# Optimization experiments

Measured on AMD Instinct MI355X. Metric: run time of the kernel, lower is better.

The kernel has to match this reference:

```python
import jax, jax.numpy as jnp
import numpy as np

THRESH = 0.1          # affinity threshold from init_kwargs
SCALES = (1, 2, 4, 8, 16)  # dyadic diffusion scales 2^0..2^4


def compute_dist(X):
    # X: [N, d] -> squared-euclidean pairwise distances via Gram matrix
    G = X @ X.T
    dg = jnp.diag(G)
    return dg[None, :] + dg[:, None] - 2.0 * G


def _diffuse(P, F):
    # returns [P^1 F, P^2 F, P^4 F, P^8 F, P^16 F] via 16 sequential applies
    outs = []
    cur = F
    for step in range(1, SCALES[-1] + 1):
        cur = P @ cur
        if step in SCALES:
            outs.append(cur)
    return outs


def _wavelet_bank(P, F):
    # lazy diffusion wavelets: psi_0 = I - P, psi_j = P^{2^{j-1}} - P^{2^j}
    lows = [F] + _diffuse(P, F)            # t = 0,1,2,4,8,16
    psis = [lows[j] - lows[j + 1] for j in range(len(lows) - 1)]  # 5 wavelets
    return psis, lows[-1]                  # (wavelet coeffs, low-pass P^16 F)


def _gwt_features(X):
    # X: [N, d] reweighted point cloud -> [N, 16*d] scattering features
    N, d = X.shape
    W = jnp.exp(-compute_dist(X) / 10.0)
    W = jnp.where(W < THRESH, jnp.zeros_like(W), W)   # sparsify affinity
    deg = W.sum(axis=1, keepdims=True)                # self-loop w=1 => deg>=1
    P = 0.5 * (jnp.eye(N, dtype=X.dtype) + W / deg)   # lazy random walk
    psis, low = _wavelet_bank(P, X)
    firsts = [jnp.abs(p) for p in psis]
    U = jnp.concatenate(firsts, axis=1)               # [N, 5*d] diffuse all at once
    psis2, _ = _wavelet_bank(P, U)
    # second order: |psi_{j2} |psi_{j1} x|| only for j2 > j1 (10 pairs)
    seconds = [jnp.abs(psis2[j2][:, : j2 * d]) for j2 in range(1, len(psis2))]
    return jnp.concatenate([low] + firsts + seconds, axis=1)  # [N, (1+5+10)*d]


def setup_inputs() -> dict:
    key = jax.random.key(0)
    k1, k2 = jax.random.split(key)
    point_clouds = jax.random.normal(k1, (4, 2048, 3), dtype=jnp.float32)
    alphas = jax.random.uniform(k2, (4, 3), dtype=jnp.float32)  # learned param
    return {"point_clouds": point_clouds, "alphas": alphas}


def reference(point_clouds, alphas):
    # point_clouds: [B, N, d]; alphas: [K, d]
    Xb = point_clouds[:, None, :, :] * alphas[None, :, None, :]  # [B, K, N, d]
    feats = jax.vmap(jax.vmap(_gwt_features))(Xb)                # [B, K, N, 16d]
    # per-cloud: cat over K along feature dim then mean over nodes == mean then flatten
    return feats.mean(axis=2).reshape(feats.shape[0], -1)        # [B, K*16*d]
```

## Files before the change

### kernel.cpp

```cpp
#include <hip/hip_runtime.h>
#include <hip/hip_bf16.h>


#define NN 2048
#define NPAIR 16

typedef _Float16 half8 __attribute__((ext_vector_type(8)));
typedef _Float16 f16x2 __attribute__((ext_vector_type(2)));
typedef float f32x4 __attribute__((ext_vector_type(4)));

extern "C" __device__ f16x2 __ocml_exp2_2f16(f16x2);

#define C2F 0.28853900817779268f
#define CWF -0.14426950408889634f
#define NL2T 3.3219280948873623f

__global__ __launch_bounds__(256) void initpack_k(const float* __restrict__ pc,
                                                  const float* __restrict__ alphas,
                                                  float* __restrict__ Xs,
                                                  _Float16* __restrict__ XT,
                                                  _Float16* __restrict__ Xp) {
    int gid = blockIdx.x * 256 + threadIdx.x;
    if (gid >= NPAIR * NN) return;
    int p = gid >> 11, i = gid & (NN - 1);
    int b = p >> 2, k = p & 3;
    const float* pcr = pc + ((size_t)b * NN + i) * 3;
    const float* al  = alphas + k * 3;
    float x = pcr[0] * al[0], y = pcr[1] * al[1], z = pcr[2] * al[2];
    float q = CWF * (x * x + y * y + z * z);
    float4 o; o.x = x; o.y = y; o.z = z; o.w = q;
    ((float4*)Xs)[gid] = o;
    _Float16* xt = XT + (size_t)p * 16 * NN + i;
    xt[0 * NN] = (_Float16)x;
    xt[1 * NN] = (_Float16)y;
    xt[2 * NN] = (_Float16)z;
    xt[3 * NN] = (_Float16)1.0f;
#pragma unroll
    for (int n = 4; n < 16; ++n) xt[n * NN] = (_Float16)0.f;
    _Float16* xp = Xp + ((size_t)p * 1024 + (i >> 1)) * 8 + (i & 1);
    xp[0] = (_Float16)x; xp[2] = (_Float16)y;
    xp[4] = (_Float16)z; xp[6] = (_Float16)q;
}

template<bool FIRST, bool BUILDU>
__global__ __launch_bounds__(512, 8)
void apply_k(const float* __restrict__ Xs, const _Float16* __restrict__ Xp,
             float* __restrict__ ihd,
             const _Float16* __restrict__ cur, _Float16* __restrict__ out,
             float* __restrict__ lvl, int t,
             const float* __restrict__ LT1u) {
    __shared__ __align__(16) float smem[4352];
    const int tid  = threadIdx.x;
    const int lane = tid & 63;
    const int wv   = tid >> 6;
    const int p    = blockIdx.y;
    const int m0   = blockIdx.x * 32;
    const int idx16 = lane & 15, quad = lane >> 4;

    {
        const float4* src = (const float4*)(Xp + (size_t)p * 8192);
        float4* dst = (float4*)smem;
        dst[tid]       = src[tid];
        dst[tid + 512] = src[tid + 512];
    }
    __syncthreads();

    f16x2 qi2[2], xx2[2], xy2[2], xz2[2];
#pragma unroll
    for (int s = 0; s < 2; ++s) {
        float4 v = *(const float4*)(Xs + ((size_t)p * NN + m0 + s * 16 + idx16) * 4);
        _Float16 q = (_Float16)(v.w + NL2T);
        _Float16 x = (_Float16)(C2F * v.x);
        _Float16 y = (_Float16)(C2F * v.y);
        _Float16 z = (_Float16)(C2F * v.z);
        qi2[s] = (f16x2){q, q}; xx2[s] = (f16x2){x, x};
        xy2[s] = (f16x2){y, y}; xz2[s] = (f16x2){z, z};
    }
    const f16x2 SC2 = (f16x2){(_Float16)32768.f, (_Float16)32768.f};

    const _Float16* bp = cur + ((size_t)p * 16 + idx16) * NN + wv * 256 + quad * 8;
    f32x4 acc[2] = {{0.f,0.f,0.f,0.f},{0.f,0.f,0.f,0.f}};

    for (int kc = 0; kc < 8; ++kc) {
        const int pb = wv * 128 + kc * 16 + quad * 4;
        half8 bf = *(const half8*)(bp + kc * 32);
        union { f16x2 h2[4]; half8 h8; } af[2];
#pragma unroll
        for (int jp = 0; jp < 4; ++jp) {
            union { float4 f; f16x2 h[4]; } e;
            e.f = ((const float4*)smem)[pb + jp];
#pragma unroll
            for (int s = 0; s < 2; ++s) {
                f16x2 tv = qi2[s] + e.h[3];
                tv = __builtin_elementwise_fma(xx2[s], e.h[0], tv);
                tv = __builtin_elementwise_fma(xy2[s], e.h[1], tv);
                tv = __builtin_elementwise_fma(xz2[s], e.h[2], tv);
                f16x2 u = __builtin_elementwise_min(tv, tv * SC2);
                af[s].h2[jp] = __ocml_exp2_2f16(u);
            }
        }
#pragma unroll
        for (int s = 0; s < 2; ++s)
            acc[s] = __builtin_amdgcn_mfma_f32_16x16x32_f16(af[s].h8, bf, acc[s], 0, 0, 0);
    }

    const int n  = tid >> 5;
    const int rr = tid & 31;
    const int s2 = rr >> 4, mloc = rr & 15;
    const int base = s2 * 256 + (mloc >> 2) * 64 + (mloc & 3);
    const int row = m0 + rr;
    float ihEff;
    if (!FIRST) ihEff = 0.1f * ihd[p * NN + row];

    __syncthreads();
#pragma unroll
    for (int s = 0; s < 2; ++s)
        *(f32x4*)&smem[wv * 512 + s * 256 + lane * 4] = acc[s];
    __syncthreads();

    float sum = 0.f;
#pragma unroll
    for (int g = 0; g < 8; ++g) sum += smem[g * 512 + base + n * 4];
    if (FIRST) {
        float deg10 = 0.f;
#pragma unroll
        for (int g = 0; g < 8; ++g) deg10 += smem[g * 512 + base + 12];
        float ih = 5.0f / deg10;
        if (n == 3) ihd[p * NN + row] = ih;
        ihEff = 0.1f * ih;
    }
    float cv = (float)cur[((size_t)p * 16 + n) * NN + row];
    float o1v = 0.5f * cv + ihEff * sum;
    if (lvl) lvl[(((size_t)p * 5 + t) * 16 + n) * NN + row] = o1v;

    if (!BUILDU) {
        out[((size_t)p * 16 + n) * NN + row] = (_Float16)o1v;
    } else {
        if (n < 3) smem[4096 + n * 32 + rr] = o1v;
        __syncthreads();
        float oval = o1v;
        if (n >= 4) {
            const int u = n - 4, jw = u / 3, c = u - 3 * jw;
            float a = (jw == 0) ? Xs[((size_t)p * NN + row) * 4 + c]
                                : LT1u[(((size_t)p * 5 + (jw - 1)) * 16 + c) * NN + row];
            float bb = (jw == 3) ? smem[4096 + c * 32 + rr]
                                 : LT1u[(((size_t)p * 5 + jw) * 16 + c) * NN + row];
            oval = fabsf(a - bb);
        }
        out[((size_t)p * 16 + n) * NN + row] = (_Float16)oval;
    }
}

__global__ __launch_bounds__(64) void reduce_k(const float* __restrict__ Xs,
                                               const float* __restrict__ LT1,
                                               const float* __restrict__ LT2,
                                               float* __restrict__ out) {
    int f = blockIdx.x, p = blockIdx.y, lane = threadIdx.x;
    const float* l1 = LT1 + (size_t)p * 5 * 16 * NN;
    const float* l2 = LT2 + (size_t)p * 5 * 16 * NN;
    float s = 0.f;
    for (int m = lane; m < NN; m += 64) {
        float v;
        if (f < 3) {
            v = l2[((size_t)3 * 16 + f) * NN + m];
        } else if (f < 18) {
            int j = (f - 3) / 3, c = (f - 3) % 3;
            float a = (j == 0) ? Xs[((size_t)p * NN + m) * 4 + c]
                               : l1[((size_t)(j - 1) * 16 + c) * NN + m];
            float b = (j < 4) ? l1[((size_t)j * 16 + c) * NN + m]
                              : l2[((size_t)3 * 16 + c) * NN + m];
            v = fabsf(a - b);
        } else {
            int gg = f - 18, j2, uc;
            if (gg < 3)       { j2 = 1; uc = gg; }
            else if (gg < 9)  { j2 = 2; uc = gg - 3; }
            else if (gg < 18) { j2 = 3; uc = gg - 9; }
            else              { j2 = 4; uc = gg - 18; }
            v = fabsf(l2[((size_t)(j2 - 1) * 16 + uc + 4) * NN + m]
                    - l2[((size_t)j2 * 16 + uc + 4) * NN + m]);
        }
        s += v;
    }
#pragma unroll
    for (int off = 32; off > 0; off >>= 1) s += __shfl_down(s, off, 64);
    if (lane == 0) out[p * 48 + f] = s * (1.0f / NN);
}

extern "C" void kernel_launch(void* const* d_in, const int* in_sizes, int n_in,
                              void* d_out, int out_size, void* d_ws, size_t ws_size,
                              hipStream_t stream) {
    const float* pc     = (const float*)d_in[0];
    const float* alphas = (const float*)d_in[1];
    float* outp = (float*)d_out;

    char* base = (char*)d_ws;
    size_t off = 0;
    auto carve = [&](size_t bytes) -> void* {
        void* r = base + off;
        off = (off + bytes + 255) & ~(size_t)255;
        return r;
    };
    float*     Xs  = (float*)carve((size_t)NPAIR * NN * 4 * sizeof(float));
    _Float16*  Xp  = (_Float16*)carve((size_t)NPAIR * 1024 * 8 * 2);
    float*     ihd = (float*)carve((size_t)NPAIR * NN * sizeof(float));
    _Float16*  XT  = (_Float16*)carve((size_t)NPAIR * 16 * NN * 2);
    _Float16*  pA  = (_Float16*)carve((size_t)NPAIR * 16 * NN * 2);
    _Float16*  pB  = (_Float16*)carve((size_t)NPAIR * 16 * NN * 2);
    float*     LT1 = (float*)carve((size_t)NPAIR * 5 * 16 * NN * sizeof(float));
    float*     LT2 = (float*)carve((size_t)NPAIR * 5 * 16 * NN * sizeof(float));

    dim3 gridA(NN / 32, NPAIR);

    initpack_k<<<dim3((NPAIR * NN) / 256), 256, 0, stream>>>(pc, alphas, Xs, XT, Xp);

    const _Float16* c1 = XT;
    int slot = 0;
    for (int step = 1; step <= 8; ++step) {
        _Float16* o1 = (c1 == pA) ? pB : pA;
        bool sv = (step & (step - 1)) == 0;
        float* lv = sv ? LT1 : nullptr;
        if (step == 1)
            apply_k<true, false><<<gridA, 512, 0, stream>>>(Xs, Xp, ihd,
                c1, o1, lv, slot, nullptr);
        else if (step == 8)
            apply_k<false, true><<<gridA, 512, 0, stream>>>(Xs, Xp, ihd,
                c1, o1, lv, slot, LT1);
        else
            apply_k<false, false><<<gridA, 512, 0, stream>>>(Xs, Xp, ihd,
                c1, o1, lv, slot, nullptr);
        if (sv) ++slot;
        c1 = o1;
    }

    int slot2 = 0;
    for (int i = 1; i <= 16; ++i) {
        _Float16* o1 = (c1 == pA) ? pB : pA;
        bool sv = (i & (i - 1)) == 0;
        float* lv = sv ? LT2 : nullptr;
        apply_k<false, false><<<gridA, 512, 0, stream>>>(Xs, Xp, ihd,
            c1, o1, lv, slot2, nullptr);
        if (sv) ++slot2;
        c1 = o1;
    }

    reduce_k<<<dim3(48, NPAIR), 64, 0, stream>>>(Xs, LT1, LT2, outp);
}
```

Measured before the change: 434.8 us.

## Materialize affinity matrix once and reuse it in subsequent diffusion applies

```diff
diff --git a/kernel.cpp b/kernel.cpp
--- a/kernel.cpp
+++ b/kernel.cpp
@@ -42,13 +42,12 @@
     xp[4] = (_Float16)z; xp[6] = (_Float16)q;
 }
 
-template<bool FIRST, bool BUILDU>
 __global__ __launch_bounds__(512, 8)
-void apply_k(const float* __restrict__ Xs, const _Float16* __restrict__ Xp,
-             float* __restrict__ ihd,
-             const _Float16* __restrict__ cur, _Float16* __restrict__ out,
-             float* __restrict__ lvl, int t,
-             const float* __restrict__ LT1u) {
+void build_apply_k(const float* __restrict__ Xs, const _Float16* __restrict__ Xp,
+                   float* __restrict__ ihd,
+                   const _Float16* __restrict__ cur, _Float16* __restrict__ out,
+                   float* __restrict__ lvl,
+                   _Float16* __restrict__ W) {
     __shared__ __align__(16) float smem[4352];
     const int tid  = threadIdx.x;
     const int lane = tid & 63;
@@ -79,6 +78,7 @@
     const f16x2 SC2 = (f16x2){(_Float16)32768.f, (_Float16)32768.f};
 
     const _Float16* bp = cur + ((size_t)p * 16 + idx16) * NN + wv * 256 + quad * 8;
+    _Float16* wp = W + ((size_t)p * NN + m0 + idx16) * NN + wv * 256 + quad * 8;
     f32x4 acc[2] = {{0.f,0.f,0.f,0.f},{0.f,0.f,0.f,0.f}};
 
     for (int kc = 0; kc < 8; ++kc) {
@@ -99,6 +99,8 @@
                 af[s].h2[jp] = __ocml_exp2_2f16(u);
             }
         }
+        *(half8*)(wp + kc * 32)                    = af[0].h8;
+        *(half8*)(wp + (size_t)16 * NN + kc * 32)  = af[1].h8;
 #pragma unroll
         for (int s = 0; s < 2; ++s)
             acc[s] = __builtin_amdgcn_mfma_f32_16x16x32_f16(af[s].h8, bf, acc[s], 0, 0, 0);
@@ -109,8 +111,6 @@
     const int s2 = rr >> 4, mloc = rr & 15;
     const int base = s2 * 256 + (mloc >> 2) * 64 + (mloc & 3);
     const int row = m0 + rr;
-    float ihEff;
-    if (!FIRST) ihEff = 0.1f * ihd[p * NN + row];
 
     __syncthreads();
 #pragma unroll
@@ -121,14 +121,61 @@
     float sum = 0.f;
 #pragma unroll
     for (int g = 0; g < 8; ++g) sum += smem[g * 512 + base + n * 4];
-    if (FIRST) {
-        float deg10 = 0.f;
-#pragma unroll
-        for (int g = 0; g < 8; ++g) deg10 += smem[g * 512 + base + 12];
-        float ih = 5.0f / deg10;
-        if (n == 3) ihd[p * NN + row] = ih;
-        ihEff = 0.1f * ih;
-    }
+    float deg10 = 0.f;
+#pragma unroll
+    for (int g = 0; g < 8; ++g) deg10 += smem[g * 512 + base + 12];
+    float ih = 5.0f / deg10;
+    if (n == 3) ihd[p * NN + row] = ih;
+    float ihEff = 0.1f * ih;
+    float cv = (float)cur[((size_t)p * 16 + n) * NN + row];
+    float o1v = 0.5f * cv + ihEff * sum;
+    lvl[(((size_t)p * 5 + 0) * 16 + n) * NN + row] = o1v;
+    out[((size_t)p * 16 + n) * NN + row] = (_Float16)o1v;
+}
+
+template<bool BUILDU>
+__global__ __launch_bounds__(512, 8)
+void gemm_apply_k(const float* __restrict__ Xs, const float* __restrict__ ihd,
+                  const _Float16* __restrict__ W,
+                  const _Float16* __restrict__ cur, _Float16* __restrict__ out,
+                  float* __restrict__ lvl, int t,
+                  const float* __restrict__ LT1u) {
+    __shared__ __align__(16) float smem[4352];
+    const int tid  = threadIdx.x;
+    const int lane = tid & 63;
+    const int wv   = tid >> 6;
+    const int p    = blockIdx.y;
+    const int m0   = blockIdx.x * 32;
+    const int idx16 = lane & 15, quad = lane >> 4;
+
+    const _Float16* bp = cur + ((size_t)p * 16 + idx16) * NN + wv * 256 + quad * 8;
+    const _Float16* wp = W + ((size_t)p * NN + m0 + idx16) * NN + wv * 256 + quad * 8;
+    f32x4 acc[2] = {{0.f,0.f,0.f,0.f},{0.f,0.f,0.f,0.f}};
+
+#pragma unroll
+    for (int kc = 0; kc < 8; ++kc) {
+        half8 bf  = *(const half8*)(bp + kc * 32);
+        half8 af0 = *(const half8*)(wp + kc * 32);
+        half8 af1 = *(const half8*)(wp + (size_t)16 * NN + kc * 32);
+        acc[0] = __builtin_amdgcn_mfma_f32_16x16x32_f16(af0, bf, acc[0], 0, 0, 0);
+        acc[1] = __builtin_amdgcn_mfma_f32_16x16x32_f16(af1, bf, acc[1], 0, 0, 0);
+    }
+
+    const int n  = tid >> 5;
+    const int rr = tid & 31;
+    const int s2 = rr >> 4, mloc = rr & 15;
+    const int base = s2 * 256 + (mloc >> 2) * 64 + (mloc & 3);
+    const int row = m0 + rr;
+    float ihEff = 0.1f * ihd[p * NN + row];
+
+#pragma unroll
+    for (int s = 0; s < 2; ++s)
+        *(f32x4*)&smem[wv * 512 + s * 256 + lane * 4] = acc[s];
+    __syncthreads();
+
+    float sum = 0.f;
+#pragma unroll
+    for (int g = 0; g < 8; ++g) sum += smem[g * 512 + base + n * 4];
     float cv = (float)cur[((size_t)p * 16 + n) * NN + row];
     float o1v = 0.5f * cv + ihEff * sum;
     if (lvl) lvl[(((size_t)p * 5 + t) * 16 + n) * NN + row] = o1v;
@@ -208,25 +255,25 @@
     _Float16*  pB  = (_Float16*)carve((size_t)NPAIR * 16 * NN * 2);
     float*     LT1 = (float*)carve((size_t)NPAIR * 5 * 16 * NN * sizeof(float));
     float*     LT2 = (float*)carve((size_t)NPAIR * 5 * 16 * NN * sizeof(float));
+    _Float16*  W   = (_Float16*)carve((size_t)NPAIR * NN * NN * 2);
 
     dim3 gridA(NN / 32, NPAIR);
 
     initpack_k<<<dim3((NPAIR * NN) / 256), 256, 0, stream>>>(pc, alphas, Xs, XT, Xp);
 
-    const _Float16* c1 = XT;
-    int slot = 0;
-    for (int step = 1; step <= 8; ++step) {
+    build_apply_k<<<gridA, 512, 0, stream>>>(Xs, Xp, ihd, XT, pA, LT1, W);
+    const _Float16* c1 = pA;
+    int slot = 1;
+
+    for (int step = 2; step <= 8; ++step) {
         _Float16* o1 = (c1 == pA) ? pB : pA;
         bool sv = (step & (step - 1)) == 0;
         float* lv = sv ? LT1 : nullptr;
-        if (step == 1)
-            apply_k<true, false><<<gridA, 512, 0, stream>>>(Xs, Xp, ihd,
-                c1, o1, lv, slot, nullptr);
-        else if (step == 8)
-            apply_k<false, true><<<gridA, 512, 0, stream>>>(Xs, Xp, ihd,
+        if (step == 8)
+            gemm_apply_k<true><<<gridA, 512, 0, stream>>>(Xs, ihd, W,
                 c1, o1, lv, slot, LT1);
         else
-            apply_k<false, false><<<gridA, 512, 0, stream>>>(Xs, Xp, ihd,
+            gemm_apply_k<false><<<gridA, 512, 0, stream>>>(Xs, ihd, W,
                 c1, o1, lv, slot, nullptr);
         if (sv) ++slot;
         c1 = o1;
@@ -237,7 +284,7 @@
         _Float16* o1 = (c1 == pA) ? pB : pA;
         bool sv = (i & (i - 1)) == 0;
         float* lv = sv ? LT2 : nullptr;
-        apply_k<false, false><<<gridA, 512, 0, stream>>>(Xs, Xp, ihd,
+        gemm_apply_k<false><<<gridA, 512, 0, stream>>>(Xs, ihd, W,
             c1, o1, lv, slot2, nullptr);
         if (sv) ++slot2;
         c1 = o1;
```

Result: slower. 654.7 us (+50.6%).

## Shrink apply tile to 16 rows, 4 waves, and read packed X directly from global

Applied to the files above, without the earlier changes.

```diff
diff --git a/kernel.cpp b/kernel.cpp
--- a/kernel.cpp
+++ b/kernel.cpp
@@ -43,91 +43,75 @@
 }
 
 template<bool FIRST, bool BUILDU>
-__global__ __launch_bounds__(512, 8)
+__global__ __launch_bounds__(256, 8)
 void apply_k(const float* __restrict__ Xs, const _Float16* __restrict__ Xp,
              float* __restrict__ ihd,
              const _Float16* __restrict__ cur, _Float16* __restrict__ out,
              float* __restrict__ lvl, int t,
              const float* __restrict__ LT1u) {
-    __shared__ __align__(16) float smem[4352];
+    __shared__ __align__(16) float smem[1088];
     const int tid  = threadIdx.x;
     const int lane = tid & 63;
     const int wv   = tid >> 6;
     const int p    = blockIdx.y;
-    const int m0   = blockIdx.x * 32;
+    const int m0   = blockIdx.x * 16;
     const int idx16 = lane & 15, quad = lane >> 4;
 
+    f16x2 qi2, xx2, xy2, xz2;
     {
-        const float4* src = (const float4*)(Xp + (size_t)p * 8192);
-        float4* dst = (float4*)smem;
-        dst[tid]       = src[tid];
-        dst[tid + 512] = src[tid + 512];
-    }
-    __syncthreads();
-
-    f16x2 qi2[2], xx2[2], xy2[2], xz2[2];
-#pragma unroll
-    for (int s = 0; s < 2; ++s) {
-        float4 v = *(const float4*)(Xs + ((size_t)p * NN + m0 + s * 16 + idx16) * 4);
+        float4 v = *(const float4*)(Xs + ((size_t)p * NN + m0 + idx16) * 4);
         _Float16 q = (_Float16)(v.w + NL2T);
         _Float16 x = (_Float16)(C2F * v.x);
         _Float16 y = (_Float16)(C2F * v.y);
         _Float16 z = (_Float16)(C2F * v.z);
-        qi2[s] = (f16x2){q, q}; xx2[s] = (f16x2){x, x};
-        xy2[s] = (f16x2){y, y}; xz2[s] = (f16x2){z, z};
+        qi2 = (f16x2){q, q}; xx2 = (f16x2){x, x};
+        xy2 = (f16x2){y, y}; xz2 = (f16x2){z, z};
     }
     const f16x2 SC2 = (f16x2){(_Float16)32768.f, (_Float16)32768.f};
 
-    const _Float16* bp = cur + ((size_t)p * 16 + idx16) * NN + wv * 256 + quad * 8;
-    f32x4 acc[2] = {{0.f,0.f,0.f,0.f},{0.f,0.f,0.f,0.f}};
-
-    for (int kc = 0; kc < 8; ++kc) {
-        const int pb = wv * 128 + kc * 16 + quad * 4;
+    const _Float16* bp = cur + ((size_t)p * 16 + idx16) * NN + wv * 512 + quad * 8;
+    const float4* Xpp = (const float4*)(Xp + (size_t)p * 8192);
+    f32x4 acc = {0.f, 0.f, 0.f, 0.f};
+
+    for (int kc = 0; kc < 16; ++kc) {
+        const int pb = wv * 256 + kc * 16 + quad * 4;
         half8 bf = *(const half8*)(bp + kc * 32);
-        union { f16x2 h2[4]; half8 h8; } af[2];
+        union { f16x2 h2[4]; half8 h8; } af;
 #pragma unroll
         for (int jp = 0; jp < 4; ++jp) {
             union { float4 f; f16x2 h[4]; } e;
-            e.f = ((const float4*)smem)[pb + jp];
-#pragma unroll
-            for (int s = 0; s < 2; ++s) {
-                f16x2 tv = qi2[s] + e.h[3];
-                tv = __builtin_elementwise_fma(xx2[s], e.h[0], tv);
-                tv = __builtin_elementwise_fma(xy2[s], e.h[1], tv);
-                tv = __builtin_elementwise_fma(xz2[s], e.h[2], tv);
-                f16x2 u = __builtin_elementwise_min(tv, tv * SC2);
-                af[s].h2[jp] = __ocml_exp2_2f16(u);
-            }
+            e.f = Xpp[pb + jp];
+            f16x2 tv = qi2 + e.h[3];
+            tv = __builtin_elementwise_fma(xx2, e.h[0], tv);
+            tv = __builtin_elementwise_fma(xy2, e.h[1], tv);
+            tv = __builtin_elementwise_fma(xz2, e.h[2], tv);
+            f16x2 u = __builtin_elementwise_min(tv, tv * SC2);
+            af.h2[jp] = __ocml_exp2_2f16(u);
         }
-#pragma unroll
-        for (int s = 0; s < 2; ++s)
-            acc[s] = __builtin_amdgcn_mfma_f32_16x16x32_f16(af[s].h8, bf, acc[s], 0, 0, 0);
-    }
-
-    const int n  = tid >> 5;
-    const int rr = tid & 31;
-    const int s2 = rr >> 4, mloc = rr & 15;
-    const int base = s2 * 256 + (mloc >> 2) * 64 + (mloc & 3);
+        acc = __builtin_amdgcn_mfma_f32_16x16x32_f16(af.h8, bf, acc, 0, 0, 0);
+    }
+
+    *(f32x4*)&smem[wv * 256 + lane * 4] = acc;
+    __syncthreads();
+
+    const int n  = tid >> 4;
+    const int rr = tid & 15;
     const int row = m0 + rr;
+    const int base = (rr >> 2) * 64 + (rr & 3);
+
+    float sum = 0.f;
+#pragma unroll
+    for (int g = 0; g < 4; ++g) sum += smem[g * 256 + base + n * 4];
     float ihEff;
-    if (!FIRST) ihEff = 0.1f * ihd[p * NN + row];
-
-    __syncthreads();
-#pragma unroll
-    for (int s = 0; s < 2; ++s)
-        *(f32x4*)&smem[wv * 512 + s * 256 + lane * 4] = acc[s];
-    __syncthreads();
-
-    float sum = 0.f;
-#pragma unroll
-    for (int g = 0; g < 8; ++g) sum += smem[g * 512 + base + n * 4];
     if (FIRST) {
         float deg10 = 0.f;
 #pragma unroll
-        for (int g = 0; g < 8; ++g) deg10 += smem[g * 512 + base + 12];
+        for (int g = 0; g < 4; ++g) deg10 += smem[g * 256 + base + 12];
         float ih = 5.0f / deg10;
         if (n == 3) ihd[p * NN + row] = ih;
         ihEff = 0.1f * ih;
+    } else {
+        ihEff = 0.1f * ihd[p * NN + row];
     }
     float cv = (float)cur[((size_t)p * 16 + n) * NN + row];
     float o1v = 0.5f * cv + ihEff * sum;
@@ -136,14 +120,14 @@
     if (!BUILDU) {
         out[((size_t)p * 16 + n) * NN + row] = (_Float16)o1v;
     } else {
-        if (n < 3) smem[4096 + n * 32 + rr] = o1v;
+        if (n < 3) smem[1024 + n * 16 + rr] = o1v;
         __syncthreads();
         float oval = o1v;
         if (n >= 4) {
             const int u = n - 4, jw = u / 3, c = u - 3 * jw;
             float a = (jw == 0) ? Xs[((size_t)p * NN + row) * 4 + c]
                                 : LT1u[(((size_t)p * 5 + (jw - 1)) * 16 + c) * NN + row];
-            float bb = (jw == 3) ? smem[4096 + c * 32 + rr]
+            float bb = (jw == 3) ? smem[1024 + c * 16 + rr]
                                  : LT1u[(((size_t)p * 5 + jw) * 16 + c) * NN + row];
             oval = fabsf(a - bb);
         }
@@ -209,7 +193,7 @@
     float*     LT1 = (float*)carve((size_t)NPAIR * 5 * 16 * NN * sizeof(float));
     float*     LT2 = (float*)carve((size_t)NPAIR * 5 * 16 * NN * sizeof(float));
 
-    dim3 gridA(NN / 32, NPAIR);
+    dim3 gridA(NN / 16, NPAIR);
 
     initpack_k<<<dim3((NPAIR * NN) / 256), 256, 0, stream>>>(pc, alphas, Xs, XT, Xp);
 
@@ -220,13 +204,13 @@
         bool sv = (step & (step - 1)) == 0;
         float* lv = sv ? LT1 : nullptr;
         if (step == 1)
-            apply_k<true, false><<<gridA, 512, 0, stream>>>(Xs, Xp, ihd,
+            apply_k<true, false><<<gridA, 256, 0, stream>>>(Xs, Xp, ihd,
                 c1, o1, lv, slot, nullptr);
         else if (step == 8)
-            apply_k<false, true><<<gridA, 512, 0, stream>>>(Xs, Xp, ihd,
+            apply_k<false, true><<<gridA, 256, 0, stream>>>(Xs, Xp, ihd,
                 c1, o1, lv, slot, LT1);
         else
-            apply_k<false, false><<<gridA, 512, 0, stream>>>(Xs, Xp, ihd,
+            apply_k<false, false><<<gridA, 256, 0, stream>>>(Xs, Xp, ihd,
                 c1, o1, lv, slot, nullptr);
         if (sv) ++slot;
         c1 = o1;
@@ -237,7 +221,7 @@
         _Float16* o1 = (c1 == pA) ? pB : pA;
         bool sv = (i & (i - 1)) == 0;
         float* lv = sv ? LT2 : nullptr;
-        apply_k<false, false><<<gridA, 512, 0, stream>>>(Xs, Xp, ihd,
+        apply_k<false, false><<<gridA, 256, 0, stream>>>(Xs, Xp, ihd,
             c1, o1, lv, slot2, nullptr);
         if (sv) ++slot2;
         c1 = o1;
```

Measured after the change: 829.4 us. +90.7%, slower.
